# Performance work log

Measured on AMD Instinct MI355X. Metric: run time of the kernel, lower is better.

The kernel has to match this reference:

```python
import jax, jax.numpy as jnp
import numpy as np

B, S, E, H, D, L, V, O = 64, 512, 512, 8, 64, 4, 50000, 1000
KW, STRIDE = 5, 5
L_OUT = (S - KW) // STRIDE + 1  # 102


def setup_inputs() -> dict:
    key = jax.random.key(0)
    ks = jax.random.split(key, 20)
    sc = 0.02
    inp = {
        'tokens': jax.random.randint(ks[0], (B, S), 0, V, dtype=jnp.int32),
        'emb': jax.random.normal(ks[1], (V + 1, E), jnp.float32) * sc,
        'Wq': jax.random.normal(ks[2], (L, H, E, D), jnp.float32) * sc,
        'bq': jnp.zeros((L, H, D), jnp.float32),
        'Wk': jax.random.normal(ks[3], (L, H, E, D), jnp.float32) * sc,
        'bk': jnp.zeros((L, H, D), jnp.float32),
        'Wv': jax.random.normal(ks[4], (L, H, E, D), jnp.float32) * sc,
        'bv': jnp.zeros((L, H, D), jnp.float32),
        'Wo': jax.random.normal(ks[5], (L, H * D, E), jnp.float32) * sc,
        'bo': jnp.zeros((L, E), jnp.float32),
        'W1': jax.random.normal(ks[6], (L, E, 2 * E), jnp.float32) * sc,
        'b1': jnp.zeros((L, 2 * E), jnp.float32),
        'W2': jax.random.normal(ks[7], (L, 2 * E, E), jnp.float32) * sc,
        'b2': jnp.zeros((L, E), jnp.float32),
        'Wc': jax.random.normal(ks[8], (KW, E, 1), jnp.float32) * sc,
        'bc': jnp.zeros((1,), jnp.float32),
        'Wd': jax.random.normal(ks[9], (L_OUT, O), jnp.float32) * sc,
        'bd': jnp.zeros((O,), jnp.float32),
    }
    return inp


def _l2_normalize(x, eps=1e-12):
    # tf.math.l2_normalize: x / sqrt(max(sum(x^2), eps))
    sq = jnp.sum(x * x, axis=-1, keepdims=True)
    return x * jax.lax.rsqrt(jnp.maximum(sq, eps))


def _forward(tokens, emb, Wq, bq, Wk, bk, Wv, bv, Wo, bo, W1, b1, W2, b2, Wc, bc, Wd, bd):
    mask = jnp.sign(tokens).astype(jnp.float32)[..., None]  # [B,S,1]
    out = emb[tokens] * mask                                 # [B,S,E]
    scale = 1.0 / jnp.sqrt(jnp.float32(E))                   # note: scaled by EMBEDDING_DIM, as in source
    for i in range(L):
        # per-head QKV projections, batched over heads
        q = jnp.einsum('bse,hed->bhsd', out, Wq[i]) + bq[i][None, :, None, :]
        k = jnp.einsum('bse,hed->bhsd', out, Wk[i]) + bk[i][None, :, None, :]
        v = jnp.einsum('bse,hed->bhsd', out, Wv[i]) + bv[i][None, :, None, :]
        scores = jnp.einsum('bhsd,bhtd->bhst', q, k) * scale
        attn = jax.nn.softmax(scores, axis=-1)
        heads = jnp.einsum('bhst,bhtd->bhsd', attn, v)       # [B,H,S,D]
        cat = heads.transpose(0, 2, 1, 3).reshape(B, S, H * D)
        mh = cat @ Wo[i] + bo[i]
        out = _l2_normalize(out + mh)
        ff = jax.nn.relu(out @ W1[i] + b1[i]) @ W2[i] + b2[i]
        out = ff + out
    # Conv1D(1, 5, strides=5) then squeeze channel, Dense over seq-length axis, softmax
    conv = jax.lax.conv_general_dilated(
        out, Wc, window_strides=(STRIDE,), padding='VALID',
        dimension_numbers=('NWC', 'WIO', 'NWC')) + bc          # [B,L_OUT,1]
    pooled = jnp.squeeze(conv, axis=-1)                        # [B,L_OUT]
    logits = pooled @ Wd + bd                                  # [B,O]
    return jax.nn.softmax(logits, axis=-1)


def reference(tokens, emb, Wq, bq, Wk, bk, Wv, bv, Wo, bo, W1, b1, W2, b2, Wc, bc, Wd, bd):
    return _forward(tokens, emb, Wq, bq, Wk, bk, Wv, bv, Wo, bo, W1, b1, W2, b2, Wc, bc, Wd, bd)
```

## Files before the change

### kernel.cpp

```cpp
#include <hip/hip_runtime.h>
#include <cstddef>

constexpr int B_ = 64, S_ = 512, E_ = 512, H_ = 8, D_ = 64, L_ = 4, O_ = 1000;
constexpr int BS_ = B_ * S_;
constexpr int HD_ = H_ * D_;
constexpr int QS_ = 1536;
constexpr int LOUT_ = 102;
constexpr float SCALE_ = 0.04419417382415922f;

typedef __bf16 bf16x8 __attribute__((ext_vector_type(8)));
typedef __bf16 bf16x4 __attribute__((ext_vector_type(4)));
typedef __bf16 bf16x2 __attribute__((ext_vector_type(2)));
typedef float floatx4 __attribute__((ext_vector_type(4)));

__device__ inline void load16_lds(const __bf16* g, __bf16* l) {
  __builtin_amdgcn_global_load_lds(
      (const __attribute__((address_space(1))) void*)g,
      (__attribute__((address_space(3))) void*)l, 16, 0, 0);
}

__global__ __launch_bounds__(256) void transpose_bf16(
    const float* __restrict__ in, __bf16* __restrict__ out,
    int R, int C, int IZ, int OZL, int OZH) {
  __shared__ float t[32][33];
  int z = blockIdx.z;
  const float* inz = in + (size_t)z * IZ;
  __bf16* outz = out + (size_t)(z >> 3) * OZL + (size_t)(z & 7) * OZH;
  int c0 = blockIdx.x * 32, r0 = blockIdx.y * 32;
  int x = threadIdx.x, y = threadIdx.y;
#pragma unroll
  for (int j = 0; j < 32; j += 8) t[y + j][x] = inz[(size_t)(r0 + y + j) * C + c0 + x];
  __syncthreads();
#pragma unroll
  for (int j = 0; j < 32; j += 8)
    outz[(size_t)(c0 + y + j) * R + r0 + x] = (__bf16)t[x][y + j];
}

__global__ __launch_bounds__(256) void bias_concat(
    const float* __restrict__ bq, const float* __restrict__ bk,
    const float* __restrict__ bv, float* __restrict__ qkvb) {
  int idx = blockIdx.x * 256 + threadIdx.x;
  int l = idx / QS_, j = idx % QS_;
  float v;
  if (j < 512) v = bq[l * 512 + j];
  else if (j < 1024) v = bk[l * 512 + j - 512];
  else v = bv[l * 512 + j - 1024];
  qkvb[idx] = v;
}

__global__ __launch_bounds__(256) void embed_kernel(
    const int* __restrict__ tokens, const float* __restrict__ emb,
    float* __restrict__ X, __bf16* __restrict__ Ab) {
  int idx = blockIdx.x * 256 + threadIdx.x;
  int bs = idx >> 7;
  int e = (idx & 127) << 2;
  int tok = tokens[bs];
  float4 v;
  if (tok == 0) v = make_float4(0.f, 0.f, 0.f, 0.f);
  else v = *(const float4*)(emb + (size_t)tok * E_ + e);
  size_t off = (size_t)bs * E_ + e;
  *(float4*)(X + off) = v;
  bf16x4 b;
  b[0] = (__bf16)v.x; b[1] = (__bf16)v.y; b[2] = (__bf16)v.z; b[3] = (__bf16)v.w;
  *(bf16x4*)(Ab + off) = b;
}

template <int RELU, int RES, int OUTF, int OUTB, int SCQ, int KT>
__global__ __launch_bounds__(256) void gemm_bf16(
    const __bf16* __restrict__ A, const __bf16* __restrict__ Bt,
    const float* __restrict__ bias, const float* __restrict__ Rsd,
    float* __restrict__ Cf, __bf16* __restrict__ Cb, int N, int lda, int Nt) {
  __shared__ __align__(16) __bf16 smem[24576];
  int tid = threadIdx.x;
  int lane = tid & 63, w = tid >> 6;
  int Mt8 = (int)(gridDim.x / Nt) >> 3;
  int xcd = blockIdx.x & 7;
  int j = blockIdx.x >> 3;
  int rr = j % (2 * Nt), chunk = j / (2 * Nt);
  int mt = xcd * Mt8 + chunk * 2 + (rr & 1);
  int nt = rr >> 1;
  int m0 = mt * 128, n0 = nt * 128;
  int q4 = lane >> 4, a_ = lane & 15;
  const int ldb = KT * 32;
  int r0s = tid >> 2, q0s = (tid & 3) ^ ((r0s >> 1) & 3);
  int r1s = 64 + (tid >> 2), q1s = (tid & 3) ^ ((r1s >> 1) & 3);
  const __bf16* Ag = A + (size_t)m0 * lda;
  const __bf16* Bg = Bt + (size_t)n0 * ldb;

  floatx4 acc[4][4];
#pragma unroll
  for (int i = 0; i < 4; ++i)
#pragma unroll
    for (int jj = 0; jj < 4; ++jj) acc[i][jj] = (floatx4)(0.0f);

  auto STAGE = [&](int kt, int bs) {
    __bf16* Ad = smem + bs * 4096;
    __bf16* Bd = smem + 12288 + bs * 4096;
    int k0 = kt * 32;
    load16_lds(Ag + (size_t)r0s * lda + k0 + q0s * 8, Ad + tid * 8);
    load16_lds(Ag + (size_t)r1s * lda + k0 + q1s * 8, Ad + (256 + tid) * 8);
    load16_lds(Bg + (size_t)r0s * ldb + k0 + q0s * 8, Bd + tid * 8);
    load16_lds(Bg + (size_t)r1s * ldb + k0 + q1s * 8, Bd + (256 + tid) * 8);
  };

  STAGE(0, 0);
  if (KT > 1) STAGE(1, 1);
#pragma unroll
  for (int kt = 0; kt < KT; ++kt) {
    if (kt + 2 < KT) {
      STAGE(kt + 2, (kt + 2) % 3);
      asm volatile("s_waitcnt vmcnt(8)" ::: "memory");
    } else if (kt + 1 < KT) {
      asm volatile("s_waitcnt vmcnt(4)" ::: "memory");
    } else {
      asm volatile("s_waitcnt vmcnt(0)" ::: "memory");
    }
    __builtin_amdgcn_s_barrier();
    __builtin_amdgcn_sched_barrier(0);
    const __bf16* As = smem + (kt % 3) * 4096;
    const __bf16* Bs = smem + 12288 + (kt % 3) * 4096;
    bf16x8 af[4], bfr[4];
#pragma unroll
    for (int i = 0; i < 4; ++i) {
      int row = (w & 1) * 64 + i * 16 + a_;
      int pc = q4 ^ ((row >> 1) & 3);
      af[i] = *(const bf16x8*)&As[(row * 4 + pc) * 8];
    }
#pragma unroll
    for (int jc = 0; jc < 4; ++jc) {
      int row = (w >> 1) * 64 + jc * 16 + a_;
      int pc = q4 ^ ((row >> 1) & 3);
      bfr[jc] = *(const bf16x8*)&Bs[(row * 4 + pc) * 8];
    }
#pragma unroll
    for (int i = 0; i < 4; ++i)
#pragma unroll
      for (int jc = 0; jc < 4; ++jc)
        acc[i][jc] = __builtin_amdgcn_mfma_f32_16x16x32_bf16(bfr[jc], af[i],
                                                             acc[i][jc], 0, 0, 0);
    asm volatile("" ::: "memory");
    __builtin_amdgcn_s_barrier();
  }
#pragma unroll
  for (int i = 0; i < 4; ++i) {
    int ml = (w & 1) * 64 + i * 16 + a_;
    int m = m0 + ml;
#pragma unroll
    for (int jc = 0; jc < 4; ++jc) {
      int nl = (w >> 1) * 64 + jc * 16 + q4 * 4;
      int n = n0 + nl;
      float4 bi = *(const float4*)(bias + n);
      floatx4 v = acc[i][jc];
      v[0] += bi.x; v[1] += bi.y; v[2] += bi.z; v[3] += bi.w;
      if (SCQ) { if (n < 512) v *= SCALE_; }
      if (RES) {
        float4 rv = *(const float4*)(Rsd + (size_t)m * N + n);
        v[0] += rv.x; v[1] += rv.y; v[2] += rv.z; v[3] += rv.w;
      }
      if (RELU) {
#pragma unroll
        for (int r = 0; r < 4; ++r) v[r] = fmaxf(v[r], 0.f);
      }
      if (OUTF) {
        float4 o = make_float4(v[0], v[1], v[2], v[3]);
        *(float4*)(Cf + (size_t)m * N + n) = o;
      }
      if (OUTB) {
        bf16x4 ob;
#pragma unroll
        for (int r = 0; r < 4; ++r) ob[r] = (__bf16)v[r];
        *(bf16x4*)&smem[ml * 136 + nl] = ob;
      }
    }
  }
  if (OUTB) {
    __syncthreads();
#pragma unroll
    for (int it = 0; it < 8; ++it) {
      int cid = it * 256 + tid;
      int row = cid >> 4, c8 = cid & 15;
      bf16x8 val = *(const bf16x8*)&smem[row * 136 + c8 * 8];
      *(bf16x8*)(Cb + (size_t)(m0 + row) * N + n0 + c8 * 8) = val;
    }
  }
}

__global__ __launch_bounds__(256, 2) void attn_bf16(__bf16* __restrict__ QKV) {
  __shared__ __align__(16) __bf16 Qs[256 * 64];
  __shared__ __align__(16) __bf16 Ks[64 * 64];
  __shared__ __align__(16) __bf16 Vt[64 * 64];
  __shared__ __align__(16) __bf16 Ps[64 * 64];
  int tid = threadIdx.x, lane = tid & 63, w = tid >> 6;
  int q4 = lane >> 4, a_ = lane & 15;
  int bid = blockIdx.x;
  int xg = bid & 7, slot = bid >> 3;
  int b = xg * 8 + (slot >> 4);
  int r_ = slot & 15;
  int h = r_ >> 1;
  int s0 = (r_ & 1) * 256;
  size_t rowbase = (size_t)b * S_ * QS_ + h * 64;
  __bf16* Qg = QKV + rowbase;
  const __bf16* Kg = QKV + rowbase + 512;
  const __bf16* Vg = QKV + rowbase + 1024;
#pragma unroll
  for (int j = 0; j < 8; ++j) {
    int ci = j * 256 + w * 64 + lane;
    int row = ci >> 3, c = ci & 7, q = c ^ (row & 7);
    load16_lds(Qg + (size_t)(s0 + row) * QS_ + q * 8, Qs + (j * 256 + w * 64) * 8);
  }
  float mrow[4], lrow[4];
  floatx4 accO[4][4];
#pragma unroll
  for (int cc = 0; cc < 4; ++cc) {
    mrow[cc] = -3.0e38f; lrow[cc] = 0.f;
#pragma unroll
    for (int jc = 0; jc < 4; ++jc) accO[cc][jc] = (floatx4)(0.0f);
  }

  for (int t0 = 0; t0 < S_; t0 += 64) {
#pragma unroll
    for (int j = 0; j < 2; ++j) {
      int ci = j * 256 + w * 64 + lane;
      int row = ci >> 3, c = ci & 7, q = c ^ (row & 7);
      load16_lds(Kg + (size_t)(t0 + row) * QS_ + q * 8, Ks + (j * 256 + w * 64) * 8);
    }
    {
      int tp = tid & 31, dg = tid >> 5;
      bf16x8 v0 = *(const bf16x8*)(Vg + (size_t)(t0 + 2 * tp) * QS_ + dg * 8);
      bf16x8 v1 = *(const bf16x8*)(Vg + (size_t)(t0 + 2 * tp + 1) * QS_ + dg * 8);
#pragma unroll
      for (int x = 0; x < 8; ++x) {
        int d = dg * 8 + x;
        bf16x2 p; p[0] = v0[x]; p[1] = v1[x];
        *(bf16x2*)&Vt[(d * 8 + ((tp >> 2) ^ (d & 7))) * 8 + (tp & 3) * 2] = p;
      }
    }
    __syncthreads();
    bf16x8 af[2][4], bv[2][4];
#pragma unroll
    for (int ks = 0; ks < 2; ++ks)
#pragma unroll
      for (int jc = 0; jc < 4; ++jc) {
        int row = jc * 16 + a_, q = ks * 4 + q4;
        af[ks][jc] = *(const bf16x8*)&Ks[(row * 8 + (q ^ (row & 7))) * 8];
        bv[ks][jc] = *(const bf16x8*)&Vt[(row * 8 + (q ^ (row & 7))) * 8];
      }
#pragma unroll
    for (int cc = 0; cc < 4; ++cc) {
      int sbase = (cc * 4 + w) * 16;
      floatx4 sc[4];
#pragma unroll
      for (int jc = 0; jc < 4; ++jc) sc[jc] = (floatx4)(0.0f);
#pragma unroll
      for (int ks = 0; ks < 2; ++ks) {
        int row = sbase + a_, q = ks * 4 + q4;
        bf16x8 bq = *(const bf16x8*)&Qs[(row * 8 + (q ^ (row & 7))) * 8];
#pragma unroll
        for (int jc = 0; jc < 4; ++jc)
          sc[jc] = __builtin_amdgcn_mfma_f32_16x16x32_bf16(af[ks][jc], bq,
                                                           sc[jc], 0, 0, 0);
      }
      float mx = sc[0][0];
#pragma unroll
      for (int jc = 0; jc < 4; ++jc)
#pragma unroll
        for (int r = 0; r < 4; ++r) mx = fmaxf(mx, sc[jc][r]);
      mx = fmaxf(mx, __shfl_xor(mx, 16));
      mx = fmaxf(mx, __shfl_xor(mx, 32));
      float mnew = fmaxf(mrow[cc], mx);
      float alpha = __expf(mrow[cc] - mnew);
      mrow[cc] = mnew;
      float ps = 0.f;
      int prow = w * 16 + a_;
#pragma unroll
      for (int jc = 0; jc < 4; ++jc) {
        bf16x4 pb;
#pragma unroll
        for (int r = 0; r < 4; ++r) {
          float p = __expf(sc[jc][r] - mnew);
          ps += p;
          pb[r] = (__bf16)p;
        }
        int pc = jc * 2 + (q4 >> 1);
        *(bf16x4*)&Ps[(prow * 8 + (pc ^ (prow & 7))) * 8 + (q4 & 1) * 4] = pb;
      }
      ps += __shfl_xor(ps, 16);
      ps += __shfl_xor(ps, 32);
      lrow[cc] = lrow[cc] * alpha + ps;
      float aal[4];
#pragma unroll
      for (int r = 0; r < 4; ++r) aal[r] = __shfl(alpha, q4 * 4 + r);
#pragma unroll
      for (int jc = 0; jc < 4; ++jc) {
        floatx4 t = accO[cc][jc];
#pragma unroll
        for (int r = 0; r < 4; ++r) t[r] *= aal[r];
        accO[cc][jc] = t;
      }
#pragma unroll
      for (int ks = 0; ks < 2; ++ks) {
        int q = ks * 4 + q4;
        bf16x8 ap = *(const bf16x8*)&Ps[(prow * 8 + (q ^ (prow & 7))) * 8];
#pragma unroll
        for (int jc = 0; jc < 4; ++jc)
          accO[cc][jc] = __builtin_amdgcn_mfma_f32_16x16x32_bf16(
              ap, bv[ks][jc], accO[cc][jc], 0, 0, 0);
      }
    }
    __syncthreads();
  }
#pragma unroll
  for (int cc = 0; cc < 4; ++cc) {
    float inv = 1.f / lrow[cc];
    float linv[4];
#pragma unroll
    for (int r = 0; r < 4; ++r) linv[r] = __shfl(inv, q4 * 4 + r);
    int srow = s0 + (cc * 4 + w) * 16 + q4 * 4;
#pragma unroll
    for (int r = 0; r < 4; ++r)
#pragma unroll
      for (int jc = 0; jc < 4; ++jc)
        Qg[(size_t)(srow + r) * QS_ + jc * 16 + a_] =
            (__bf16)(accO[cc][jc][r] * linv[r]);
  }
}

__global__ __launch_bounds__(256) void addnorm_kernel(
    float* __restrict__ X, const __bf16* __restrict__ MH, __bf16* __restrict__ Ab) {
  int row = blockIdx.x * 4 + (threadIdx.x >> 6);
  int ln = threadIdx.x & 63;
  size_t off = (size_t)row * E_ + ln * 8;
  float xv[8];
  *(float4*)&xv[0] = *(const float4*)(X + off);
  *(float4*)&xv[4] = *(const float4*)(X + off + 4);
  bf16x8 mh = *(const bf16x8*)(MH + off);
  float ss = 0.f;
#pragma unroll
  for (int j = 0; j < 8; ++j) {
    xv[j] += (float)mh[j];
    ss += xv[j] * xv[j];
  }
#pragma unroll
  for (int o = 1; o < 64; o <<= 1) ss += __shfl_xor(ss, o);
  float inv = rsqrtf(fmaxf(ss, 1e-12f));
  bf16x8 ob;
#pragma unroll
  for (int j = 0; j < 8; ++j) {
    xv[j] *= inv;
    ob[j] = (__bf16)xv[j];
  }
  *(float4*)(X + off) = *(float4*)&xv[0];
  *(float4*)(X + off + 4) = *(float4*)&xv[4];
  *(bf16x8*)(Ab + off) = ob;
}

__global__ __launch_bounds__(256) void conv_pool_kernel(
    const float* __restrict__ X, const float* __restrict__ Wc,
    const float* __restrict__ bc, float* __restrict__ pooled) {
  int wid = blockIdx.x * 4 + (threadIdx.x >> 6);
  int ln = threadIdx.x & 63;
  int b = wid / LOUT_, l = wid % LOUT_;
  const float* xr = X + (size_t)b * S_ * E_ + (size_t)l * 5 * E_;
  float v = 0.f;
#pragma unroll
  for (int j = 0; j < 10; ++j) {
    int i = (j * 64 + ln) * 4;
    float4 x4 = *(const float4*)(xr + i);
    float4 w4 = *(const float4*)(Wc + i);
    v += x4.x * w4.x + x4.y * w4.y + x4.z * w4.z + x4.w * w4.w;
  }
#pragma unroll
  for (int o = 32; o >= 1; o >>= 1) v += __shfl_down(v, o);
  if (ln == 0) pooled[b * LOUT_ + l] = v + bc[0];
}

__global__ __launch_bounds__(256) void dense_softmax_kernel(
    const float* __restrict__ pooled, const float* __restrict__ Wd,
    const float* __restrict__ bd, float* __restrict__ out) {
  __shared__ float pl[LOUT_];
  __shared__ float red[256];
  __shared__ float lg[O_];
  int b = blockIdx.x, tid = threadIdx.x;
  if (tid < LOUT_) pl[tid] = pooled[b * LOUT_ + tid];
  __syncthreads();
  for (int o = tid; o < O_; o += 256) {
    float acc = bd[o];
#pragma unroll 6
    for (int l = 0; l < LOUT_; ++l) acc += pl[l] * Wd[l * O_ + o];
    lg[o] = acc;
  }
  __syncthreads();
  float mx = -3.0e38f;
  for (int o = tid; o < O_; o += 256) mx = fmaxf(mx, lg[o]);
  red[tid] = mx;
  __syncthreads();
  for (int s2 = 128; s2 > 0; s2 >>= 1) {
    if (tid < s2) red[tid] = fmaxf(red[tid], red[tid + s2]);
    __syncthreads();
  }
  mx = red[0];
  __syncthreads();
  float se = 0.f;
  for (int o = tid; o < O_; o += 256) {
    float e = __expf(lg[o] - mx);
    lg[o] = e;
    se += e;
  }
  red[tid] = se;
  __syncthreads();
  for (int s2 = 128; s2 > 0; s2 >>= 1) {
    if (tid < s2) red[tid] += red[tid + s2];
    __syncthreads();
  }
  float inv = 1.f / red[0];
  for (int o = tid; o < O_; o += 256) out[(size_t)b * O_ + o] = lg[o] * inv;
}

extern "C" void kernel_launch(void* const* d_in, const int* in_sizes, int n_in,
                              void* d_out, int out_size, void* d_ws, size_t ws_size,
                              hipStream_t stream) {
  const int* tokens = (const int*)d_in[0];
  const float* emb = (const float*)d_in[1];
  const float* Wq = (const float*)d_in[2];
  const float* bq = (const float*)d_in[3];
  const float* Wk = (const float*)d_in[4];
  const float* bk = (const float*)d_in[5];
  const float* Wv = (const float*)d_in[6];
  const float* bv = (const float*)d_in[7];
  const float* Wo = (const float*)d_in[8];
  const float* bo = (const float*)d_in[9];
  const float* W1 = (const float*)d_in[10];
  const float* b1 = (const float*)d_in[11];
  const float* W2 = (const float*)d_in[12];
  const float* b2 = (const float*)d_in[13];
  const float* Wc = (const float*)d_in[14];
  const float* bc = (const float*)d_in[15];
  const float* Wd = (const float*)d_in[16];
  const float* bd = (const float*)d_in[17];
  float* out = (float*)d_out;

  char* ws = (char*)d_ws;
  float* X = (float*)ws;
  __bf16* Ab = (__bf16*)(ws + 67108864);
  __bf16* QKVb = (__bf16*)(ws + 100663296);
  __bf16* FF1b = QKVb;
  __bf16* MHb = (__bf16*)(ws + 201326592);
  __bf16* Wt = (__bf16*)(ws + 234881024);
  __bf16* Wt_qkv = Wt;
  __bf16* Wt_o = Wt + 3145728;
  __bf16* Wt_1 = Wt + 4194304;
  __bf16* Wt_2 = Wt + 6291456;
  float* qkvbias = (float*)(ws + 251658240);
  float* pooled = qkvbias + 6144;

  dim3 tb(32, 8);
  transpose_bf16<<<dim3(2, 16, 32), tb, 0, stream>>>(Wq, Wt_qkv + 0,      512, 64, 32768, 786432, 32768);
  transpose_bf16<<<dim3(2, 16, 32), tb, 0, stream>>>(Wk, Wt_qkv + 262144, 512, 64, 32768, 786432, 32768);
  transpose_bf16<<<dim3(2, 16, 32), tb, 0, stream>>>(Wv, Wt_qkv + 524288, 512, 64, 32768, 786432, 32768);
  transpose_bf16<<<dim3(16, 16, 4), tb, 0, stream>>>(Wo, Wt_o, 512, 512, 262144, 0, 262144);
  transpose_bf16<<<dim3(32, 16, 4), tb, 0, stream>>>(W1, Wt_1, 512, 1024, 524288, 0, 524288);
  transpose_bf16<<<dim3(16, 32, 4), tb, 0, stream>>>(W2, Wt_2, 1024, 512, 524288, 0, 524288);
  bias_concat<<<dim3(24), dim3(256), 0, stream>>>(bq, bk, bv, qkvbias);

  embed_kernel<<<dim3(BS_ * E_ / 4 / 256), dim3(256), 0, stream>>>(tokens, emb, X, Ab);

  dim3 blk(256);
  for (int i = 0; i < L_; ++i) {
    gemm_bf16<0, 0, 0, 1, 1, 16><<<dim3(256 * 12), blk, 0, stream>>>(
        Ab, Wt_qkv + (size_t)i * 786432, qkvbias + i * QS_, nullptr, nullptr,
        QKVb, QS_, 512, 12);
    attn_bf16<<<dim3(1024), blk, 0, stream>>>(QKVb);
    gemm_bf16<0, 0, 0, 1, 0, 16><<<dim3(256 * 4), blk, 0, stream>>>(
        QKVb, Wt_o + (size_t)i * 262144, bo + i * E_, nullptr, nullptr, MHb,
        512, QS_, 4);
    addnorm_kernel<<<dim3(BS_ / 4), blk, 0, stream>>>(X, MHb, Ab);
    gemm_bf16<1, 0, 0, 1, 0, 16><<<dim3(256 * 8), blk, 0, stream>>>(
        Ab, Wt_1 + (size_t)i * 524288, b1 + (size_t)i * 2 * E_, nullptr, nullptr,
        FF1b, 1024, 512, 8);
    gemm_bf16<0, 1, 1, 1, 0, 32><<<dim3(256 * 4), blk, 0, stream>>>(
        FF1b, Wt_2 + (size_t)i * 524288, b2 + (size_t)i * E_, X, X, Ab,
        512, 1024, 4);
  }
  conv_pool_kernel<<<dim3(BS_ * LOUT_ / S_ / 4), blk, 0, stream>>>(X, Wc, bc, pooled);
  dense_softmax_kernel<<<dim3(B_), blk, 0, stream>>>(pooled, Wd, bd, out);
}
```

Before: 1.383 ms.

## Double-buffer K/V tiles in attention kernel to overlap loads with compute

The attention kernel now keeps two LDS buffers for K and transposed V and prefetches the next 64-row K tile (async global-to-LDS) and V registers while computing on the current tile. Barriers are replaced by explicit s_waitcnt plus s_barrier so that outstanding prefetches are not drained each iteration. This aims to hide global memory latency in the inner loop. In exchange it uses more LDS (16KB more), which may reduce occupancy, and the hand-written vmcnt counts are fragile.

Result: no change. 1.391 ms (+0.6%).

```diff
diff --git a/kernel.cpp b/kernel.cpp
--- a/kernel.cpp
+++ b/kernel.cpp
@@ -187,8 +187,8 @@
 
 __global__ __launch_bounds__(256, 2) void attn_bf16(__bf16* __restrict__ QKV) {
   __shared__ __align__(16) __bf16 Qs[256 * 64];
-  __shared__ __align__(16) __bf16 Ks[64 * 64];
-  __shared__ __align__(16) __bf16 Vt[64 * 64];
+  __shared__ __align__(16) __bf16 Ks[2][64 * 64];
+  __shared__ __align__(16) __bf16 Vt[2][64 * 64];
   __shared__ __align__(16) __bf16 Ps[64 * 64];
   int tid = threadIdx.x, lane = tid & 63, w = tid >> 6;
   int q4 = lane >> 4, a_ = lane & 15;
@@ -208,6 +208,16 @@
     int row = ci >> 3, c = ci & 7, q = c ^ (row & 7);
     load16_lds(Qg + (size_t)(s0 + row) * QS_ + q * 8, Qs + (j * 256 + w * 64) * 8);
   }
+#pragma unroll
+  for (int j = 0; j < 2; ++j) {
+    int ci = j * 256 + w * 64 + lane;
+    int row = ci >> 3, c = ci & 7, q = c ^ (row & 7);
+    load16_lds(Kg + (size_t)row * QS_ + q * 8, &Ks[0][(j * 256 + w * 64) * 8]);
+  }
+  int tp = tid & 31, dg = tid >> 5;
+  bf16x8 v0 = *(const bf16x8*)(Vg + (size_t)(2 * tp) * QS_ + dg * 8);
+  bf16x8 v1 = *(const bf16x8*)(Vg + (size_t)(2 * tp + 1) * QS_ + dg * 8);
+
   float mrow[4], lrow[4];
   floatx4 accO[4][4];
 #pragma unroll
@@ -217,33 +227,42 @@
     for (int jc = 0; jc < 4; ++jc) accO[cc][jc] = (floatx4)(0.0f);
   }
 
-  for (int t0 = 0; t0 < S_; t0 += 64) {
-#pragma unroll
-    for (int j = 0; j < 2; ++j) {
-      int ci = j * 256 + w * 64 + lane;
-      int row = ci >> 3, c = ci & 7, q = c ^ (row & 7);
-      load16_lds(Kg + (size_t)(t0 + row) * QS_ + q * 8, Ks + (j * 256 + w * 64) * 8);
-    }
-    {
-      int tp = tid & 31, dg = tid >> 5;
-      bf16x8 v0 = *(const bf16x8*)(Vg + (size_t)(t0 + 2 * tp) * QS_ + dg * 8);
-      bf16x8 v1 = *(const bf16x8*)(Vg + (size_t)(t0 + 2 * tp + 1) * QS_ + dg * 8);
-#pragma unroll
-      for (int x = 0; x < 8; ++x) {
-        int d = dg * 8 + x;
-        bf16x2 p; p[0] = v0[x]; p[1] = v1[x];
-        *(bf16x2*)&Vt[(d * 8 + ((tp >> 2) ^ (d & 7))) * 8 + (tp & 3) * 2] = p;
-      }
-    }
-    __syncthreads();
+  for (int t = 0; t < 8; ++t) {
+    int t0 = t * 64;
+    int cur = t & 1;
+    if (t + 1 < 8) {
+#pragma unroll
+      for (int j = 0; j < 2; ++j) {
+        int ci = j * 256 + w * 64 + lane;
+        int row = ci >> 3, c = ci & 7, q = c ^ (row & 7);
+        load16_lds(Kg + (size_t)(t0 + 64 + row) * QS_ + q * 8,
+                   &Ks[cur ^ 1][(j * 256 + w * 64) * 8]);
+      }
+      asm volatile("s_waitcnt vmcnt(2)" ::: "memory");
+    } else {
+      asm volatile("s_waitcnt vmcnt(0)" ::: "memory");
+    }
+#pragma unroll
+    for (int x = 0; x < 8; ++x) {
+      int d = dg * 8 + x;
+      bf16x2 p; p[0] = v0[x]; p[1] = v1[x];
+      *(bf16x2*)&Vt[cur][(d * 8 + ((tp >> 2) ^ (d & 7))) * 8 + (tp & 3) * 2] = p;
+    }
+    if (t + 1 < 8) {
+      v0 = *(const bf16x8*)(Vg + (size_t)(t0 + 64 + 2 * tp) * QS_ + dg * 8);
+      v1 = *(const bf16x8*)(Vg + (size_t)(t0 + 64 + 2 * tp + 1) * QS_ + dg * 8);
+    }
+    asm volatile("s_waitcnt lgkmcnt(0)" ::: "memory");
+    __builtin_amdgcn_s_barrier();
+    asm volatile("" ::: "memory");
     bf16x8 af[2][4], bv[2][4];
 #pragma unroll
     for (int ks = 0; ks < 2; ++ks)
 #pragma unroll
       for (int jc = 0; jc < 4; ++jc) {
         int row = jc * 16 + a_, q = ks * 4 + q4;
-        af[ks][jc] = *(const bf16x8*)&Ks[(row * 8 + (q ^ (row & 7))) * 8];
-        bv[ks][jc] = *(const bf16x8*)&Vt[(row * 8 + (q ^ (row & 7))) * 8];
+        af[ks][jc] = *(const bf16x8*)&Ks[cur][(row * 8 + (q ^ (row & 7))) * 8];
+        bv[ks][jc] = *(const bf16x8*)&Vt[cur][(row * 8 + (q ^ (row & 7))) * 8];
       }
 #pragma unroll
     for (int cc = 0; cc < 4; ++cc) {
@@ -292,10 +311,10 @@
       for (int r = 0; r < 4; ++r) aal[r] = __shfl(alpha, q4 * 4 + r);
 #pragma unroll
       for (int jc = 0; jc < 4; ++jc) {
-        floatx4 t = accO[cc][jc];
-#pragma unroll
-        for (int r = 0; r < 4; ++r) t[r] *= aal[r];
-        accO[cc][jc] = t;
+        floatx4 tt = accO[cc][jc];
+#pragma unroll
+        for (int r = 0; r < 4; ++r) tt[r] *= aal[r];
+        accO[cc][jc] = tt;
       }
 #pragma unroll
       for (int ks = 0; ks < 2; ++ks) {
@@ -307,7 +326,9 @@
               ap, bv[ks][jc], accO[cc][jc], 0, 0, 0);
       }
     }
-    __syncthreads();
+    asm volatile("" ::: "memory");
+    __builtin_amdgcn_s_barrier();
+    asm volatile("" ::: "memory");
   }
 #pragma unroll
   for (int cc = 0; cc < 4; ++cc) {
```

## Fuse output projection GEMM with residual add and L2 normalize

Applied to the files above, without the earlier changes.

Adds a dedicated GEMM kernel for the Wo projection in which each block owns 64 full rows (all 512 output columns), so the epilogue can add bias and residual, reduce row sums of squares across waves via shared memory, and write the normalized fp32 X and bf16 copy directly. This replaces the separate Wo GEMM plus addnorm kernel and removes the bf16 MH round trip through global memory. In exchange the grid shrinks to 512 blocks with 72KB of dynamic shared memory and a heavy register footprint, which may reduce occupancy and latency hiding compared with the narrower-tile GEMM.

Measured after the change: 1.377 ms. Within noise of the previous version (-0.4%).

```diff
diff --git a/kernel.cpp b/kernel.cpp
--- a/kernel.cpp
+++ b/kernel.cpp
@@ -185,6 +185,126 @@
   }
 }
 
+__global__ __launch_bounds__(256) void gemm_wo_addnorm(
+    const __bf16* __restrict__ A, const __bf16* __restrict__ Bt,
+    const float* __restrict__ bias, float* __restrict__ X,
+    __bf16* __restrict__ Ab) {
+  extern __shared__ __align__(16) __bf16 smem[];
+  __bf16* As0 = smem;
+  __bf16* Bs0 = smem + 4096;
+  int tid = threadIdx.x;
+  int lane = tid & 63, w = tid >> 6;
+  int q4 = lane >> 4, a_ = lane & 15;
+  int xcd = blockIdx.x & 7;
+  int mt = xcd * 64 + (blockIdx.x >> 3);
+  int m0 = mt * 64;
+  const int lda = QS_, ldb = 512, N = 512;
+  int ra = tid >> 2, qa = (tid & 3) ^ ((ra >> 1) & 3);
+  const __bf16* Ag = A + (size_t)m0 * lda;
+
+  floatx4 acc[4][8];
+#pragma unroll
+  for (int i = 0; i < 4; ++i)
+#pragma unroll
+    for (int jj = 0; jj < 8; ++jj) acc[i][jj] = (floatx4)(0.0f);
+
+  auto STAGE = [&](int t, int s) {
+    int k0 = t * 32;
+    load16_lds(Ag + (size_t)ra * lda + k0 + qa * 8, As0 + s * 2048 + tid * 8);
+#pragma unroll
+    for (int k = 0; k < 8; ++k) {
+      int ci = k * 256 + tid;
+      int row = ci >> 2, q = (ci & 3) ^ ((row >> 1) & 3);
+      load16_lds(Bt + (size_t)row * ldb + k0 + q * 8, Bs0 + s * 16384 + ci * 8);
+    }
+  };
+
+  STAGE(0, 0);
+#pragma unroll
+  for (int t = 0; t < 16; ++t) {
+    if (t + 1 < 16) {
+      STAGE(t + 1, (t + 1) & 1);
+      asm volatile("s_waitcnt vmcnt(9)" ::: "memory");
+    } else {
+      asm volatile("s_waitcnt vmcnt(0)" ::: "memory");
+    }
+    __builtin_amdgcn_s_barrier();
+    __builtin_amdgcn_sched_barrier(0);
+    const __bf16* As = As0 + (t & 1) * 2048;
+    const __bf16* Bs = Bs0 + (t & 1) * 16384;
+    bf16x8 af[4], bfr[8];
+#pragma unroll
+    for (int mf = 0; mf < 4; ++mf) {
+      int row = mf * 16 + a_;
+      af[mf] = *(const bf16x8*)&As[(row * 4 + (q4 ^ ((row >> 1) & 3))) * 8];
+    }
+#pragma unroll
+    for (int nf = 0; nf < 8; ++nf) {
+      int row = w * 128 + nf * 16 + a_;
+      bfr[nf] = *(const bf16x8*)&Bs[(row * 4 + (q4 ^ ((row >> 1) & 3))) * 8];
+    }
+#pragma unroll
+    for (int mf = 0; mf < 4; ++mf)
+#pragma unroll
+      for (int nf = 0; nf < 8; ++nf)
+        acc[mf][nf] = __builtin_amdgcn_mfma_f32_16x16x32_bf16(bfr[nf], af[mf],
+                                                              acc[mf][nf], 0, 0, 0);
+    asm volatile("" ::: "memory");
+    __builtin_amdgcn_s_barrier();
+  }
+
+  float* sq = (float*)smem;
+  __bf16* Cs = smem + 2048;
+  float persq[4];
+#pragma unroll
+  for (int mf = 0; mf < 4; ++mf) {
+    persq[mf] = 0.f;
+    int m = m0 + mf * 16 + a_;
+#pragma unroll
+    for (int nf = 0; nf < 8; ++nf) {
+      int n = w * 128 + nf * 16 + q4 * 4;
+      float4 bi = *(const float4*)(bias + n);
+      float4 xo = *(const float4*)(X + (size_t)m * N + n);
+      floatx4 v = acc[mf][nf];
+      v[0] += bi.x + xo.x; v[1] += bi.y + xo.y;
+      v[2] += bi.z + xo.z; v[3] += bi.w + xo.w;
+      acc[mf][nf] = v;
+      persq[mf] += v[0] * v[0] + v[1] * v[1] + v[2] * v[2] + v[3] * v[3];
+    }
+    persq[mf] += __shfl_xor(persq[mf], 16);
+    persq[mf] += __shfl_xor(persq[mf], 32);
+    if (q4 == 0) sq[w * 64 + mf * 16 + a_] = persq[mf];
+  }
+  __syncthreads();
+#pragma unroll
+  for (int mf = 0; mf < 4; ++mf) {
+    int rowl = mf * 16 + a_;
+    float s = sq[rowl] + sq[64 + rowl] + sq[128 + rowl] + sq[192 + rowl];
+    float inv = rsqrtf(fmaxf(s, 1e-12f));
+    int m = m0 + rowl;
+#pragma unroll
+    for (int nf = 0; nf < 8; ++nf) {
+      int nl = w * 128 + nf * 16 + q4 * 4;
+      floatx4 v = acc[mf][nf];
+      float4 o;
+      o.x = v[0] * inv; o.y = v[1] * inv; o.z = v[2] * inv; o.w = v[3] * inv;
+      *(float4*)(X + (size_t)m * N + nl) = o;
+      bf16x4 ob;
+      ob[0] = (__bf16)o.x; ob[1] = (__bf16)o.y;
+      ob[2] = (__bf16)o.z; ob[3] = (__bf16)o.w;
+      *(bf16x4*)&Cs[rowl * 520 + nl] = ob;
+    }
+  }
+  __syncthreads();
+#pragma unroll
+  for (int it = 0; it < 16; ++it) {
+    int cid = it * 256 + tid;
+    int row = cid >> 6, c8 = cid & 63;
+    bf16x8 val = *(const bf16x8*)&Cs[row * 520 + c8 * 8];
+    *(bf16x8*)(Ab + (size_t)(m0 + row) * N + c8 * 8) = val;
+  }
+}
+
 __global__ __launch_bounds__(256, 2) void attn_bf16(__bf16* __restrict__ QKV) {
   __shared__ __align__(16) __bf16 Qs[256 * 64];
   __shared__ __align__(16) __bf16 Ks[64 * 64];
@@ -323,35 +443,6 @@
         Qg[(size_t)(srow + r) * QS_ + jc * 16 + a_] =
             (__bf16)(accO[cc][jc][r] * linv[r]);
   }
-}
-
-__global__ __launch_bounds__(256) void addnorm_kernel(
-    float* __restrict__ X, const __bf16* __restrict__ MH, __bf16* __restrict__ Ab) {
-  int row = blockIdx.x * 4 + (threadIdx.x >> 6);
-  int ln = threadIdx.x & 63;
-  size_t off = (size_t)row * E_ + ln * 8;
-  float xv[8];
-  *(float4*)&xv[0] = *(const float4*)(X + off);
-  *(float4*)&xv[4] = *(const float4*)(X + off + 4);
-  bf16x8 mh = *(const bf16x8*)(MH + off);
-  float ss = 0.f;
-#pragma unroll
-  for (int j = 0; j < 8; ++j) {
-    xv[j] += (float)mh[j];
-    ss += xv[j] * xv[j];
-  }
-#pragma unroll
-  for (int o = 1; o < 64; o <<= 1) ss += __shfl_xor(ss, o);
-  float inv = rsqrtf(fmaxf(ss, 1e-12f));
-  bf16x8 ob;
-#pragma unroll
-  for (int j = 0; j < 8; ++j) {
-    xv[j] *= inv;
-    ob[j] = (__bf16)xv[j];
-  }
-  *(float4*)(X + off) = *(float4*)&xv[0];
-  *(float4*)(X + off + 4) = *(float4*)&xv[4];
-  *(bf16x8*)(Ab + off) = ob;
 }
 
 __global__ __launch_bounds__(256) void conv_pool_kernel(
@@ -444,7 +535,6 @@
   __bf16* Ab = (__bf16*)(ws + 67108864);
   __bf16* QKVb = (__bf16*)(ws + 100663296);
   __bf16* FF1b = QKVb;
-  __bf16* MHb = (__bf16*)(ws + 201326592);
   __bf16* Wt = (__bf16*)(ws + 234881024);
   __bf16* Wt_qkv = Wt;
   __bf16* Wt_o = Wt + 3145728;
@@ -452,6 +542,10 @@
   __bf16* Wt_2 = Wt + 6291456;
   float* qkvbias = (float*)(ws + 251658240);
   float* pooled = qkvbias + 6144;
+
+  constexpr int WOSMEM = 73728;
+  hipFuncSetAttribute((const void*)gemm_wo_addnorm,
+                      hipFuncAttributeMaxDynamicSharedMemorySize, WOSMEM);
 
   dim3 tb(32, 8);
   transpose_bf16<<<dim3(2, 16, 32), tb, 0, stream>>>(Wq, Wt_qkv + 0,      512, 64, 32768, 786432, 32768);
@@ -470,10 +564,8 @@
         Ab, Wt_qkv + (size_t)i * 786432, qkvbias + i * QS_, nullptr, nullptr,
         QKVb, QS_, 512, 12);
     attn_bf16<<<dim3(1024), blk, 0, stream>>>(QKVb);
-    gemm_bf16<0, 0, 0, 1, 0, 16><<<dim3(256 * 4), blk, 0, stream>>>(
-        QKVb, Wt_o + (size_t)i * 262144, bo + i * E_, nullptr, nullptr, MHb,
-        512, QS_, 4);
-    addnorm_kernel<<<dim3(BS_ / 4), blk, 0, stream>>>(X, MHb, Ab);
+    gemm_wo_addnorm<<<dim3(512), blk, WOSMEM, stream>>>(
+        QKVb, Wt_o + (size_t)i * 262144, bo + i * E_, X, Ab);
     gemm_bf16<1, 0, 0, 1, 0, 16><<<dim3(256 * 8), blk, 0, stream>>>(
         Ab, Wt_1 + (size_t)i * 524288, b1 + (size_t)i * 2 * E_, nullptr, nullptr,
         FF1b, 1024, 512, 8);
```
